# Optimization experiments

Measured on AMD Instinct MI355X. Metric: run time of the kernel, lower is better.

The kernel has to match this reference:

```python
import jax, jax.numpy as jnp
import numpy as np

N_USERS = 50000
N_ENT = 100000
N_EDGES = 2_000_000
N_INTER = 1_000_000
CHANNEL = 64
N_HEADS = 2
D_K = CHANNEL // N_HEADS
N_HOPS = 2
N_REL = 10  # relation_emb has N_REL-1 rows


def setup_inputs() -> dict:
    key = jax.random.key(0)
    ks = jax.random.split(key, 8)
    user_emb = jax.random.normal(ks[0], (N_USERS, CHANNEL), jnp.float32) * 0.1
    entity_emb = jax.random.normal(ks[1], (N_ENT, CHANNEL), jnp.float32) * 0.1
    relation_emb = jax.random.normal(ks[2], (N_REL - 1, CHANNEL), jnp.float32) * 0.1
    W_Q = jax.random.normal(ks[3], (CHANNEL, CHANNEL), jnp.float32) * (1.0 / np.sqrt(CHANNEL))
    edge_index = jax.random.randint(ks[4], (2, N_EDGES), 0, N_ENT)
    edge_type = jax.random.randint(ks[5], (N_EDGES,), 1, N_REL)  # in [1, N_REL-1]
    inter_edge = jnp.stack([
        jax.random.randint(ks[6], (N_INTER,), 0, N_USERS),
        jax.random.randint(ks[7], (N_INTER,), 0, N_ENT),
    ])
    inter_edge_w = jnp.full((N_INTER,), 1.0 / 20.0, jnp.float32)
    return {
        "user_emb": user_emb,
        "entity_emb": entity_emb,
        "relation_emb": relation_emb,
        "W_Q": W_Q,
        "inter_edge_w": inter_edge_w,
        "edge_index": edge_index,
        "edge_type": edge_type,
        "inter_edge": inter_edge,
    }


def _l2norm(x):
    # F.normalize(dim=-1) with eps=1e-12
    n = jnp.linalg.norm(x, axis=-1, keepdims=True)
    return x / jnp.maximum(n, 1e-12)


def _scatter_softmax(logits, seg, num_segments):
    # per-segment (over leading axis) numerically-stable softmax; logits [E, H]
    m = jax.ops.segment_max(logits, seg, num_segments=num_segments)
    e = jnp.exp(logits - m[seg])
    s = jax.ops.segment_sum(e, seg, num_segments=num_segments)
    return e / s[seg]


def reference(user_emb, entity_emb, relation_emb, W_Q, inter_edge_w,
              edge_index, edge_type, inter_edge):
    head, tail = edge_index[0], edge_index[1]
    u_idx, i_idx = inter_edge[0], inter_edge[1]
    rel = relation_emb[edge_type - 1]  # [E, C]
    inv_sqrt_dk = 1.0 / np.sqrt(D_K)

    entity_res, user_res = entity_emb, user_emb
    for _ in range(N_HOPS):
        h_emb = entity_emb[head]                       # [E, C]
        t_emb = entity_emb[tail]                       # [E, C]
        q = (h_emb @ W_Q).reshape(-1, N_HEADS, D_K)    # [E, H, Dk]
        k = (t_emb @ W_Q).reshape(-1, N_HEADS, D_K) * rel.reshape(-1, N_HEADS, D_K)
        score = (q * k).sum(-1) * inv_sqrt_dk          # [E, H]
        attn = _scatter_softmax(score, head, N_ENT)    # [E, H]
        value = (t_emb * rel).reshape(-1, N_HEADS, D_K)
        agg = (value * attn[..., None]).reshape(-1, CHANNEL)
        entity_agg = jax.ops.segment_sum(agg, head, num_segments=N_ENT)
        item_agg = inter_edge_w[:, None] * entity_emb[i_idx]
        user_agg = jax.ops.segment_sum(item_agg, u_idx, num_segments=N_USERS)
        # mess_dropout disabled (eval mode)
        entity_emb = _l2norm(entity_agg)
        user_emb = _l2norm(user_agg)
        entity_res = entity_res + entity_emb
        user_res = user_res + user_emb
    return entity_res, user_res
```

## Files before the change

### kernel.cpp

```cpp
#include <hip/hip_runtime.h>

#define NU     50000
#define NEN    100000
#define NEDGE  2000000
#define NINTER 1000000
#define CH     64
#define NRELM1 9
#define CAPE   64
#define CAPU   64

#define BINSH   8
#define NBINE   ((NEN + 255) >> BINSH)
#define NBINU   ((NU  + 255) >> BINSH)
#define CHUNKE  8192
#define CHUNKU  4096
#define NBE_BLK ((NEDGE  + CHUNKE - 1) / CHUNKE)
#define NBU_BLK ((NINTER + CHUNKU - 1) / CHUNKU)
#define DSTRE   416
#define DSTRU   224
#define NSTR_E  ((NEN * CH) / 2048)
#define NSTR_U  ((NU * CH + 2047) / 2048)
#define NPLACE  (NBINE + NBINU)
#define NGEMM   ((NEN + 63) / 64)

typedef _Float16 hv2 __attribute__((ext_vector_type(2)));
typedef _Float16 h8  __attribute__((ext_vector_type(8)));
typedef float    f32x4 __attribute__((ext_vector_type(4)));
union P4 { float4 f; hv2 h[4]; };

static __device__ __forceinline__ hv2 pkrtz(float a, float b) {
    return __builtin_bit_cast(hv2, __builtin_amdgcn_cvt_pkrtz(a, b));
}


__global__ __launch_bounds__(256) void k_bin(
    const float* __restrict__ ue, const float* __restrict__ ee,
    const float* __restrict__ re, const float* __restrict__ wq,
    const float* __restrict__ iw, const int* __restrict__ eidx,
    const int* __restrict__ etype, const int* __restrict__ ii,
    _Float16* __restrict__ QE, float* __restrict__ Eres, float* __restrict__ Ures,
    _Float16* __restrict__ Relh, _Float16* __restrict__ Wt,
    unsigned* __restrict__ dirE, unsigned* __restrict__ dirU,
    int* __restrict__ blkBufE, unsigned long long* __restrict__ blkBufU)
{
    __shared__ long long srt64[CHUNKU];
    __shared__ int hist[512];
    __shared__ int sc[512];
    int* srt = (int*)srt64;
    int b = blockIdx.x, tid = threadIdx.x;

    if (b < NBE_BLK) {
        hist[tid] = 0; hist[tid + 256] = 0;
        __syncthreads();
        int base = b * CHUNKE;
        int n = NEDGE - base; if (n > CHUNKE) n = CHUNKE;
        for (int i = tid; i < n; i += 256)
            atomicAdd(&hist[eidx[base + i] >> BINSH], 1);
        __syncthreads();
        sc[tid] = hist[tid]; sc[tid + 256] = hist[tid + 256];
        __syncthreads();
#pragma unroll
        for (int off = 1; off < 512; off <<= 1) {
            int v0 = (tid >= off) ? sc[tid - off] : 0;
            int v1 = sc[tid + 256 - off];
            __syncthreads();
            sc[tid] += v0; sc[tid + 256] += v1;
            __syncthreads();
        }
        sc[tid] -= hist[tid]; sc[tid + 256] -= hist[tid + 256];
        __syncthreads();
        for (int i = tid; i < n; i += 256) {
            int h  = eidx[base + i];
            int t  = eidx[NEDGE + base + i];
            int rt = etype[base + i] - 1;
            int pos = atomicAdd(&sc[h >> BINSH], 1);
            srt[pos] = (h & 255) | ((t | (rt << 17)) << 8);
        }
        __syncthreads();
        int4* dst = (int4*)(blkBufE + b * CHUNKE);
        const int4* s4 = (const int4*)srt;
        for (int j = tid; j < ((n + 3) >> 2); j += 256) dst[j] = s4[j];
        for (int bin = tid; bin < NBINE; bin += 256)
            dirE[b * DSTRE + bin] =
                ((unsigned)(sc[bin] - hist[bin]) << 16) | (unsigned)hist[bin];
    } else if (b < NBE_BLK + NBU_BLK) {
        hist[tid] = 0; hist[tid + 256] = 0;
        __syncthreads();
        int ub = b - NBE_BLK;
        int base = ub * CHUNKU;
        int n = NINTER - base; if (n > CHUNKU) n = CHUNKU;
        for (int i = tid; i < n; i += 256)
            atomicAdd(&hist[ii[base + i] >> BINSH], 1);
        __syncthreads();
        sc[tid] = hist[tid]; sc[tid + 256] = hist[tid + 256];
        __syncthreads();
#pragma unroll
        for (int off = 1; off < 512; off <<= 1) {
            int v0 = (tid >= off) ? sc[tid - off] : 0;
            int v1 = sc[tid + 256 - off];
            __syncthreads();
            sc[tid] += v0; sc[tid + 256] += v1;
            __syncthreads();
        }
        sc[tid] -= hist[tid]; sc[tid + 256] -= hist[tid + 256];
        __syncthreads();
        for (int i = tid; i < n; i += 256) {
            int u = ii[base + i];
            int e = ii[NINTER + base + i];
            unsigned w = __float_as_uint(iw[base + i]);
            int pos = atomicAdd(&sc[u >> BINSH], 1);
            srt64[pos] = (unsigned long long)((u & 255) | (e << 8))
                       | ((unsigned long long)w << 32);
        }
        __syncthreads();
        int4* dst = (int4*)(blkBufU + (size_t)ub * CHUNKU);
        const int4* s4 = (const int4*)srt64;
        for (int j = tid; j < ((n + 1) >> 1); j += 256) dst[j] = s4[j];
        for (int bin = tid; bin < NBINU; bin += 256)
            dirU[ub * DSTRU + bin] =
                ((unsigned)(sc[bin] - hist[bin]) << 16) | (unsigned)hist[bin];
    } else {
        int sb = b - (NBE_BLK + NBU_BLK);
        if (sb < NSTR_E) {
            int i0 = sb * 2048 + tid * 8;
            float4 a = *(const float4*)(ee + i0);
            float4 c = *(const float4*)(ee + i0 + 4);
            *(float4*)(Eres + i0)     = a;
            *(float4*)(Eres + i0 + 4) = c;
            P4 o;
            o.h[0] = pkrtz(a.x, a.y);
            o.h[1] = pkrtz(a.z, a.w);
            o.h[2] = pkrtz(c.x, c.y);
            o.h[3] = pkrtz(c.z, c.w);
            int node = i0 >> 6, c0 = i0 & 63;
            *(float4*)(QE + (size_t)node * 128 + c0) = o.f;
        } else if (sb < NSTR_E + NSTR_U) {
            int i0 = (sb - NSTR_E) * 2048 + tid * 8;
            if (i0 < NU * CH) {
                *(float4*)(Ures + i0)     = *(const float4*)(ue + i0);
                *(float4*)(Ures + i0 + 4) = *(const float4*)(ue + i0 + 4);
            }
        } else {
            for (int i = tid; i < NRELM1 * CH; i += 256)
                Relh[i] = (_Float16)re[i];
            for (int i = tid; i < CH * CH; i += 256)
                Wt[(i & 63) * 64 + (i >> 6)] = (_Float16)wq[i];
        }
    }
}

__global__ __launch_bounds__(256) void k_pg(
    const unsigned* __restrict__ dirE, const int* __restrict__ blkBufE,
    const unsigned* __restrict__ dirU, const unsigned long long* __restrict__ blkBufU,
    int* __restrict__ cntE, int* __restrict__ csrE,
    int* __restrict__ cntU, unsigned long long* __restrict__ csrU2,
    _Float16* __restrict__ QE, const _Float16* __restrict__ Wt)
{
    __shared__ int cnt[256];
    int b = blockIdx.x, tid = threadIdx.x;
    if (b >= NPLACE) {
        int gb = b - NPLACE;
        int w = tid >> 6, lane = tid & 63;
        int r0 = gb * 64 + w * 16;
        if (r0 >= NEN) return;
        int lr = lane & 15, lg = lane >> 4;
        const _Float16* arow = QE + (size_t)(r0 + lr) * 128 + lg * 8;
        h8 a0 = *(const h8*)(arow);
        h8 a1 = *(const h8*)(arow + 32);
#pragma unroll
        for (int ct = 0; ct < 4; ++ct) {
            const _Float16* brow = Wt + (ct * 16 + lr) * 64 + lg * 8;
            h8 b0 = *(const h8*)(brow);
            h8 b1 = *(const h8*)(brow + 32);
            f32x4 c = {0.f, 0.f, 0.f, 0.f};
            c = __builtin_amdgcn_mfma_f32_16x16x32_f16(a0, b0, c, 0, 0, 0);
            c = __builtin_amdgcn_mfma_f32_16x16x32_f16(a1, b1, c, 0, 0, 0);
#pragma unroll
            for (int r = 0; r < 4; ++r)
                QE[(size_t)(r0 + lg * 4 + r) * 128 + 64 + ct * 16 + lr] = (_Float16)c[r];
        }
        return;
    }
    cnt[tid] = 0;
    __syncthreads();
    if (b < NBINE) {
        if (tid < NBE_BLK) {
            unsigned d = dirE[tid * DSTRE + b];
            int off = d >> 16, c = d & 0xFFFF;
            const int* src = blkBufE + tid * CHUNKE + off;
            for (int i = 0; i < c; ++i) {
                int rec = src[i];
                int nl = rec & 255;
                int pos = atomicAdd(&cnt[nl], 1);
                if (pos < CAPE) csrE[((b << BINSH) + nl) * CAPE + pos] = rec >> 8;
            }
        }
        __syncthreads();
        int node = (b << BINSH) + tid;
        if (node < NEN) { int c = cnt[tid]; cntE[node] = c > CAPE ? CAPE : c; }
    } else {
        int ub = b - NBINE;
        if (tid < NBU_BLK) {
            unsigned d = dirU[tid * DSTRU + ub];
            int off = d >> 16, c = d & 0xFFFF;
            const unsigned long long* src = blkBufU + (size_t)tid * CHUNKU + off;
            for (int i = 0; i < c; ++i) {
                unsigned long long rec = src[i];
                int nl = (int)rec & 255;
                int pos = atomicAdd(&cnt[nl], 1);
                if (pos < CAPU)
                    csrU2[((ub << BINSH) + nl) * CAPU + pos] =
                        ((rec & 0xFFFFFFFFull) >> 8) | (rec & 0xFFFFFFFF00000000ull);
            }
        }
        __syncthreads();
        int node = (ub << BINSH) + tid;
        if (node < NU) { int c = cnt[tid]; cntU[node] = c > CAPU ? CAPU : c; }
    }
}

__global__ __launch_bounds__(256) void k_gemm(
    _Float16* __restrict__ QE, const _Float16* __restrict__ Wt)
{
    int w = threadIdx.x >> 6, lane = threadIdx.x & 63;
    int r0 = blockIdx.x * 64 + w * 16;
    if (r0 >= NEN) return;
    int lr = lane & 15, lg = lane >> 4;
    const _Float16* arow = QE + (size_t)(r0 + lr) * 128 + lg * 8;
    h8 a0 = *(const h8*)(arow);
    h8 a1 = *(const h8*)(arow + 32);
#pragma unroll
    for (int ct = 0; ct < 4; ++ct) {
        const _Float16* brow = Wt + (ct * 16 + lr) * 64 + lg * 8;
        h8 b0 = *(const h8*)(brow);
        h8 b1 = *(const h8*)(brow + 32);
        f32x4 c = {0.f, 0.f, 0.f, 0.f};
        c = __builtin_amdgcn_mfma_f32_16x16x32_f16(a0, b0, c, 0, 0, 0);
        c = __builtin_amdgcn_mfma_f32_16x16x32_f16(a1, b1, c, 0, 0, 0);
#pragma unroll
        for (int r = 0; r < 4; ++r)
            QE[(size_t)(r0 + lg * 4 + r) * 128 + 64 + ct * 16 + lr] = (_Float16)c[r];
    }
}

template<bool LAST>
__global__ __launch_bounds__(256) void k_fused(
    const int* __restrict__ cntE, const int* __restrict__ csrE,
    const _Float16* __restrict__ QE, const _Float16* __restrict__ Relh,
    _Float16* __restrict__ QEn, float* __restrict__ Eres,
    const int* __restrict__ cntU, const unsigned long long* __restrict__ csrU2,
    float* __restrict__ Ures)
{
    __shared__ __attribute__((aligned(16))) _Float16 RelL[NRELM1 * 72];
    int tid = threadIdx.x;
    if (tid < 72) *(float4*)(RelL + (tid >> 3) * 72 + (tid & 7) * 8)
                      = *(const float4*)(Relh + tid * 8);
    __syncthreads();

    int pair = blockIdx.x * 4 + (tid >> 6);
    int lane = tid & 63;
    int wid  = pair * 2 + (lane >> 5);
    int s = (lane >> 3) & 3, l = lane & 7;
    int c8 = l * 8;

    if (wid < NEN) {
        int row = wid;
        int cnt = cntE[row];
        int beg = row * CAPE, end = beg + cnt;
        P4 q; q.f = *(const float4*)(QE + (size_t)row * 128 + 64 + c8);
        float acc[8] = {0.f,0.f,0.f,0.f,0.f,0.f,0.f,0.f};
        float den = 0.f;

        int a0 = beg + s;
        int iA = (a0 < end) ? csrE[a0] : 0;
        int iB = (a0 + 4 < end) ? csrE[a0 + 4] : 0;
        P4 teA, ktA, rlA;
        {
            const _Float16* bA = QE + (size_t)(iA & 0x1FFFF) * 128 + c8;
            teA.f = *(const float4*)bA;
            ktA.f = *(const float4*)(bA + 64);
            rlA.f = *(const float4*)(RelL + (iA >> 17) * 72 + c8);
        }
        int nit = (cnt + 3) >> 2;
        for (int it = 0; it < nit; ++it) {
            P4 teB, ktB, rlB;
            {
                const _Float16* bB = QE + (size_t)(iB & 0x1FFFF) * 128 + c8;
                teB.f = *(const float4*)bB;
                ktB.f = *(const float4*)(bB + 64);
                rlB.f = *(const float4*)(RelL + (iB >> 17) * 72 + c8);
            }
            int a2 = a0 + (it + 2) * 4;
            int iN = (a2 < end) ? csrE[a2] : 0;
            bool act = (a0 + it * 4) < end;
            float sc = 0.f;
#pragma unroll
            for (int i = 0; i < 4; ++i) {
                hv2 km = ktA.h[i] * rlA.h[i];
                sc = __builtin_amdgcn_fdot2(q.h[i], km, sc, false);
            }
            sc += __shfl_xor(sc, 1);
            sc += __shfl_xor(sc, 2);
            float ex = exp2f(sc * 0.25503489f);
            if (!act) ex = 0.f;
            den += ex;
#pragma unroll
            for (int i = 0; i < 4; ++i) {
                hv2 vm = teA.h[i] * rlA.h[i];
                acc[2*i]   += ex * (float)vm.x;
                acc[2*i+1] += ex * (float)vm.y;
            }
            teA = teB; ktA = ktB; rlA = rlB; iB = iN;
        }
        hv2 pk[4];
#pragma unroll
        for (int i = 0; i < 4; ++i)
            pk[i] = pkrtz(acc[2*i], acc[2*i+1]);
#pragma unroll
        for (int m = 8; m <= 16; m <<= 1) {
#pragma unroll
            for (int i = 0; i < 4; ++i) {
                int v = __shfl_xor(__builtin_bit_cast(int, pk[i]), m);
                pk[i] += __builtin_bit_cast(hv2, v);
            }
            den += __shfl_xor(den, m);
        }
        float af[8];
#pragma unroll
        for (int i = 0; i < 4; ++i) { af[2*i] = (float)pk[i].x; af[2*i+1] = (float)pk[i].y; }
        float invd = (den > 0.f) ? 1.f / den : 0.f;
        float ss = 0.f;
#pragma unroll
        for (int k = 0; k < 8; ++k) { af[k] *= invd; ss += af[k] * af[k]; }
        ss += __shfl_xor(ss, 1); ss += __shfl_xor(ss, 2); ss += __shfl_xor(ss, 4);
        float inv = 1.f / fmaxf(sqrtf(ss), 1e-12f);
#pragma unroll
        for (int k = 0; k < 8; ++k) af[k] *= inv;
        if (s == 0) {
            if (!LAST) {
                P4 o;
#pragma unroll
                for (int i = 0; i < 4; ++i)
                    o.h[i] = pkrtz(af[2*i], af[2*i+1]);
                *(float4*)(QEn + (size_t)row * 128 + c8) = o.f;
            }
            float4 r0 = *(const float4*)(Eres + (size_t)row * 64 + c8);
            float4 r1 = *(const float4*)(Eres + (size_t)row * 64 + c8 + 4);
            r0.x += af[0]; r0.y += af[1]; r0.z += af[2]; r0.w += af[3];
            r1.x += af[4]; r1.y += af[5]; r1.z += af[6]; r1.w += af[7];
            *(float4*)(Eres + (size_t)row * 64 + c8)     = r0;
            *(float4*)(Eres + (size_t)row * 64 + c8 + 4) = r1;
        }
    } else {
        int row = wid - NEN;
        int cnt = cntU[row];
        int beg = row * CAPU, end = beg + cnt;
        float acc[8] = {0.f,0.f,0.f,0.f,0.f,0.f,0.f,0.f};
        int a0 = beg + s;
        unsigned long long recA = (a0 < end) ? csrU2[a0] : 0ull;
        unsigned long long recB = (a0 + 4 < end) ? csrU2[a0 + 4] : 0ull;
        P4 teA; teA.f = *(const float4*)(QE + (size_t)(unsigned)recA * 128 + c8);
        int nit = (cnt + 3) >> 2;
        for (int it = 0; it < nit; ++it) {
            P4 teB; teB.f = *(const float4*)(QE + (size_t)(unsigned)recB * 128 + c8);
            int a2 = a0 + (it + 2) * 4;
            unsigned long long recN = (a2 < end) ? csrU2[a2] : 0ull;
            float wA = __uint_as_float((unsigned)(recA >> 32));
#pragma unroll
            for (int i = 0; i < 4; ++i) {
                acc[2*i]   += wA * (float)teA.h[i].x;
                acc[2*i+1] += wA * (float)teA.h[i].y;
            }
            teA = teB; recA = recB; recB = recN;
        }
        hv2 pk[4];
#pragma unroll
        for (int i = 0; i < 4; ++i)
            pk[i] = pkrtz(acc[2*i], acc[2*i+1]);
#pragma unroll
        for (int m = 8; m <= 16; m <<= 1) {
#pragma unroll
            for (int i = 0; i < 4; ++i) {
                int v = __shfl_xor(__builtin_bit_cast(int, pk[i]), m);
                pk[i] += __builtin_bit_cast(hv2, v);
            }
        }
        float af[8];
#pragma unroll
        for (int i = 0; i < 4; ++i) { af[2*i] = (float)pk[i].x; af[2*i+1] = (float)pk[i].y; }
        float ss = 0.f;
#pragma unroll
        for (int k = 0; k < 8; ++k) ss += af[k] * af[k];
        ss += __shfl_xor(ss, 1); ss += __shfl_xor(ss, 2); ss += __shfl_xor(ss, 4);
        float inv = 1.f / fmaxf(sqrtf(ss), 1e-12f);
        if (s == 0) {
            float4 r0 = *(const float4*)(Ures + (size_t)row * 64 + c8);
            float4 r1 = *(const float4*)(Ures + (size_t)row * 64 + c8 + 4);
            r0.x += af[0] * inv; r0.y += af[1] * inv; r0.z += af[2] * inv; r0.w += af[3] * inv;
            r1.x += af[4] * inv; r1.y += af[5] * inv; r1.z += af[6] * inv; r1.w += af[7] * inv;
            *(float4*)(Ures + (size_t)row * 64 + c8)     = r0;
            *(float4*)(Ures + (size_t)row * 64 + c8 + 4) = r1;
        }
    }
}

extern "C" void kernel_launch(void* const* d_in, const int* in_sizes, int n_in,
                              void* d_out, int out_size, void* d_ws, size_t ws_size,
                              hipStream_t stream)
{
    const float* ue = (const float*)d_in[0];
    const float* ee = (const float*)d_in[1];
    const float* re = (const float*)d_in[2];
    const float* wq = (const float*)d_in[3];
    const float* iw = (const float*)d_in[4];
    const int* eidx  = (const int*)d_in[5];
    const int* etype = (const int*)d_in[6];
    const int* ii    = (const int*)d_in[7];

    float* Eres = (float*)d_out;
    float* Ures = Eres + (size_t)NEN * CH;

    _Float16* Relh = (_Float16*)d_ws;
    _Float16* Wt   = Relh + 1024;
    _Float16* QEA  = Wt + 4096;
    _Float16* QEB  = QEA + (size_t)NEN * 128;
    int* cntE      = (int*)(QEB + (size_t)NEN * 128);
    int* cntU      = cntE + NEN;
    int* csrE      = cntU + NU;
    unsigned long long* csrU2 = (unsigned long long*)(csrE + (size_t)NEN * CAPE);
    unsigned* dirE = (unsigned*)(csrU2 + (size_t)NU * CAPU);
    unsigned* dirU = dirE + NBE_BLK * DSTRE;
    int* blkBufE   = (int*)QEB;
    unsigned long long* blkBufU =
        (unsigned long long*)((char*)QEB + (size_t)NBE_BLK * CHUNKE * 4);

    k_bin<<<NBE_BLK + NBU_BLK + NSTR_E + NSTR_U + 1, 256, 0, stream>>>(
        ue, ee, re, wq, iw, eidx, etype, ii,
        QEA, Eres, Ures, Relh, Wt, dirE, dirU, blkBufE, blkBufU);
    k_pg<<<NPLACE + NGEMM, 256, 0, stream>>>(dirE, blkBufE, dirU, blkBufU,
                                             cntE, csrE, cntU, csrU2, QEA, Wt);
    k_fused<false><<<(NEN + NU) / 8, 256, 0, stream>>>(cntE, csrE, QEA, Relh,
                                                       QEB, Eres, cntU, csrU2, Ures);
    k_gemm<<<NGEMM, 256, 0, stream>>>(QEB, Wt);
    k_fused<true><<<(NEN + NU) / 8, 256, 0, stream>>>(cntE, csrE, QEB, Relh,
                                                      QEA, Eres, cntU, csrU2, Ures);
}
```

Before: 419.1 us.

## Halve binning chunks, widen placement blocks, and use wave-shuffle prefix scan

The edge and interaction binning chunks are halved, which doubles the number of source blocks. The placement kernel moves to 512 threads so each thread walks a shorter serial per-bin record list, with twice as many threads per bin sharing that work. The shared-memory Hillis-Steele scan in the binning kernel is replaced by a wave-level shuffle scan plus a small cross-wave fixup, cutting the number of block barriers. The fused GEMM part of the placement kernel now covers 128 rows per block. In exchange there are more directory entries and more binning blocks to launch, and the directory buffer grows, which relies on the workspace being large enough.

```diff
diff --git a/kernel.cpp b/kernel.cpp
--- a/kernel.cpp
+++ b/kernel.cpp
@@ -12,8 +12,8 @@
 #define BINSH   8
 #define NBINE   ((NEN + 255) >> BINSH)
 #define NBINU   ((NU  + 255) >> BINSH)
-#define CHUNKE  8192
-#define CHUNKU  4096
+#define CHUNKE  4096
+#define CHUNKU  2048
 #define NBE_BLK ((NEDGE  + CHUNKE - 1) / CHUNKE)
 #define NBU_BLK ((NINTER + CHUNKU - 1) / CHUNKU)
 #define DSTRE   416
@@ -21,6 +21,7 @@
 #define NSTR_E  ((NEN * CH) / 2048)
 #define NSTR_U  ((NU * CH + 2047) / 2048)
 #define NPLACE  (NBINE + NBINU)
+#define NGEMM0  ((NEN + 127) / 128)
 #define NGEMM   ((NEN + 63) / 64)
 
 typedef _Float16 hv2 __attribute__((ext_vector_type(2)));
@@ -46,8 +47,10 @@
     __shared__ long long srt64[CHUNKU];
     __shared__ int hist[512];
     __shared__ int sc[512];
+    __shared__ int segtot[8];
     int* srt = (int*)srt64;
     int b = blockIdx.x, tid = threadIdx.x;
+    int lane63 = tid & 63, wv = tid >> 6;
 
     if (b < NBE_BLK) {
         hist[tid] = 0; hist[tid + 256] = 0;
@@ -57,18 +60,28 @@
         for (int i = tid; i < n; i += 256)
             atomicAdd(&hist[eidx[base + i] >> BINSH], 1);
         __syncthreads();
-        sc[tid] = hist[tid]; sc[tid + 256] = hist[tid + 256];
-        __syncthreads();
-#pragma unroll
-        for (int off = 1; off < 512; off <<= 1) {
-            int v0 = (tid >= off) ? sc[tid - off] : 0;
-            int v1 = sc[tid + 256 - off];
+        {
+            int v0 = hist[tid], v1 = hist[tid + 256];
+            int s0 = v0, s1 = v1;
+#pragma unroll
+            for (int off = 1; off < 64; off <<= 1) {
+                int u0 = __shfl_up(s0, off);
+                int u1 = __shfl_up(s1, off);
+                if (lane63 >= off) { s0 += u0; s1 += u1; }
+            }
+            if (lane63 == 63) { segtot[wv] = s0; segtot[4 + wv] = s1; }
             __syncthreads();
-            sc[tid] += v0; sc[tid + 256] += v1;
+            int base0 = 0, base1 = 0;
+#pragma unroll
+            for (int k = 0; k < 8; ++k) {
+                int t = segtot[k];
+                if (k < wv)     base0 += t;
+                if (k < 4 + wv) base1 += t;
+            }
+            sc[tid]       = base0 + s0 - v0;
+            sc[tid + 256] = base1 + s1 - v1;
             __syncthreads();
         }
-        sc[tid] -= hist[tid]; sc[tid + 256] -= hist[tid + 256];
-        __syncthreads();
         for (int i = tid; i < n; i += 256) {
             int h  = eidx[base + i];
             int t  = eidx[NEDGE + base + i];
@@ -92,18 +105,28 @@
         for (int i = tid; i < n; i += 256)
             atomicAdd(&hist[ii[base + i] >> BINSH], 1);
         __syncthreads();
-        sc[tid] = hist[tid]; sc[tid + 256] = hist[tid + 256];
-        __syncthreads();
-#pragma unroll
-        for (int off = 1; off < 512; off <<= 1) {
-            int v0 = (tid >= off) ? sc[tid - off] : 0;
-            int v1 = sc[tid + 256 - off];
+        {
+            int v0 = hist[tid], v1 = hist[tid + 256];
+            int s0 = v0, s1 = v1;
+#pragma unroll
+            for (int off = 1; off < 64; off <<= 1) {
+                int u0 = __shfl_up(s0, off);
+                int u1 = __shfl_up(s1, off);
+                if (lane63 >= off) { s0 += u0; s1 += u1; }
+            }
+            if (lane63 == 63) { segtot[wv] = s0; segtot[4 + wv] = s1; }
             __syncthreads();
-            sc[tid] += v0; sc[tid + 256] += v1;
+            int base0 = 0, base1 = 0;
+#pragma unroll
+            for (int k = 0; k < 8; ++k) {
+                int t = segtot[k];
+                if (k < wv)     base0 += t;
+                if (k < 4 + wv) base1 += t;
+            }
+            sc[tid]       = base0 + s0 - v0;
+            sc[tid + 256] = base1 + s1 - v1;
             __syncthreads();
         }
-        sc[tid] -= hist[tid]; sc[tid + 256] -= hist[tid + 256];
-        __syncthreads();
         for (int i = tid; i < n; i += 256) {
             int u = ii[base + i];
             int e = ii[NINTER + base + i];
@@ -149,7 +172,7 @@
     }
 }
 
-__global__ __launch_bounds__(256) void k_pg(
+__global__ __launch_bounds__(512) void k_pg(
     const unsigned* __restrict__ dirE, const int* __restrict__ blkBufE,
     const unsigned* __restrict__ dirU, const unsigned long long* __restrict__ blkBufU,
     int* __restrict__ cntE, int* __restrict__ csrE,
@@ -161,7 +184,7 @@
     if (b >= NPLACE) {
         int gb = b - NPLACE;
         int w = tid >> 6, lane = tid & 63;
-        int r0 = gb * 64 + w * 16;
+        int r0 = gb * 128 + w * 16;
         if (r0 >= NEN) return;
         int lr = lane & 15, lg = lane >> 4;
         const _Float16* arow = QE + (size_t)(r0 + lr) * 128 + lg * 8;
@@ -181,7 +204,7 @@
         }
         return;
     }
-    cnt[tid] = 0;
+    if (tid < 256) cnt[tid] = 0;
     __syncthreads();
     if (b < NBINE) {
         if (tid < NBE_BLK) {
@@ -196,8 +219,10 @@
             }
         }
         __syncthreads();
-        int node = (b << BINSH) + tid;
-        if (node < NEN) { int c = cnt[tid]; cntE[node] = c > CAPE ? CAPE : c; }
+        if (tid < 256) {
+            int node = (b << BINSH) + tid;
+            if (node < NEN) { int c = cnt[tid]; cntE[node] = c > CAPE ? CAPE : c; }
+        }
     } else {
         int ub = b - NBINE;
         if (tid < NBU_BLK) {
@@ -214,8 +239,10 @@
             }
         }
         __syncthreads();
-        int node = (ub << BINSH) + tid;
-        if (node < NU) { int c = cnt[tid]; cntU[node] = c > CAPU ? CAPU : c; }
+        if (tid < 256) {
+            int node = (ub << BINSH) + tid;
+            if (node < NU) { int c = cnt[tid]; cntU[node] = c > CAPU ? CAPU : c; }
+        }
     }
 }
 
@@ -437,8 +464,8 @@
     k_bin<<<NBE_BLK + NBU_BLK + NSTR_E + NSTR_U + 1, 256, 0, stream>>>(
         ue, ee, re, wq, iw, eidx, etype, ii,
         QEA, Eres, Ures, Relh, Wt, dirE, dirU, blkBufE, blkBufU);
-    k_pg<<<NPLACE + NGEMM, 256, 0, stream>>>(dirE, blkBufE, dirU, blkBufU,
-                                             cntE, csrE, cntU, csrU2, QEA, Wt);
+    k_pg<<<NPLACE + NGEMM0, 512, 0, stream>>>(dirE, blkBufE, dirU, blkBufU,
+                                              cntE, csrE, cntU, csrU2, QEA, Wt);
     k_fused<false><<<(NEN + NU) / 8, 256, 0, stream>>>(cntE, csrE, QEA, Relh,
                                                        QEB, Eres, cntU, csrU2, Ures);
     k_gemm<<<NGEMM, 256, 0, stream>>>(QEB, Wt);
```

New measurement: 407.6 us, median of 2. 2.7% less time.
